# Performance work log

Measured on AMD Instinct MI355X. Metric: run time of the kernel, lower is better.

## Reference

```python
import jax, jax.numpy as jnp
import numpy as np

N = 100000   # num_nodes
E = 1600000  # num_edges (avg degree 16)
D = 64       # embed_channels
C = 16       # num_classes
EPSILON = 0.1  # AntiSymmetricConv step size (PyG default)
GAMMA = 0.1    # AntiSymmetricConv diffusion strength (PyG default)


def setup_inputs() -> dict:
    key = jax.random.key(0)
    ks = jax.random.split(key, 9)
    s = 1.0 / np.sqrt(D)
    return {
        "edge_index": jax.random.randint(ks[0], (2, E), 0, N, dtype=jnp.int32),
        "embed_w": jax.random.normal(ks[1], (N, D), dtype=jnp.float32) * 0.1,
        "W_rel": jax.random.normal(ks[2], (D, D), dtype=jnp.float32) * s,   # GraphConv lin_rel weight
        "b_rel": jax.random.normal(ks[3], (D,), dtype=jnp.float32) * s,     # GraphConv lin_rel bias
        "W_root": jax.random.normal(ks[4], (D, D), dtype=jnp.float32) * s,  # GraphConv lin_root weight (no bias)
        "W_anti": jax.random.normal(ks[5], (D, D), dtype=jnp.float32) * s,  # AntiSymmetricConv W
        "b_anti": jax.random.normal(ks[6], (D,), dtype=jnp.float32) * s,    # AntiSymmetricConv bias
        "W_lin": jax.random.normal(ks[7], (C, D), dtype=jnp.float32) * s,   # lin2 weight
        "b_lin": jax.random.normal(ks[8], (C,), dtype=jnp.float32) * s,     # lin2 bias
    }


def reference(edge_index, embed_w, W_rel, b_rel, W_root, W_anti, b_anti, W_lin, b_lin):
    x = embed_w  # [N, D] node features = embedding table
    src, dst = edge_index[0], edge_index[1]
    # phi = GraphConv with 'add' aggregation: lin_rel(sum_j x_j) + lin_root(x)
    agg = jax.ops.segment_sum(x[src], dst, num_segments=N)  # [N, D] sparse gather+scatter-add
    h = agg @ W_rel.T + b_rel + x @ W_root.T
    # antisymmetric weight: W - W^T - gamma * I
    aW = W_anti - W_anti.T - GAMMA * jnp.eye(D, dtype=x.dtype)
    h = x @ aW.T + h + b_anti
    h = jnp.tanh(h)                       # default act of AntiSymmetricConv
    x = x + EPSILON * h                   # single iteration (num_iters=1 default)
    # dropout p=0.0 -> identity
    out = jax.nn.sigmoid(x @ W_lin.T + b_lin)  # [N, C]
    return out
```

## Files before the change

kernel.cpp:

```cpp
#include <hip/hip_runtime.h>

#define DD 64
#define CC 16
#define EPSILON 0.1f
#define GAMMA 0.1f
#define BSH 6
#define BSZ 64
#define CAP 1280
#define MAXBK 2048
#define PAD 65
#define PADW 65
#define CSH 10
#define MAXNC 128
#define CAPC 20480
#define L1CHUNK 2048
#define L1THR 512
#define NSLICE 8
#define SRTSZ 2560

typedef float v2f __attribute__((ext_vector_type(2)));

__global__ __launch_bounds__(L1THR) void bin_coarse_conv(
        const int* __restrict__ ei, int* __restrict__ gcntc,
        unsigned* __restrict__ binned_c, int E,
        const float* __restrict__ x, unsigned* __restrict__ x_q, int N) {
    __shared__ unsigned sorted[SRTSZ];
    __shared__ unsigned char bkt[SRTSZ];
    __shared__ int hist[MAXNC], ph[MAXNC], base[MAXNC], cur[MAXNC], gbase[MAXNC];
    __shared__ int mtot;
    const int t = threadIdx.x;
    if (t < MAXNC) hist[t] = 0;
    __syncthreads();
    const int e0 = blockIdx.x * L1CHUNK;
    unsigned ent[L1CHUNK / L1THR];
    int cbk[L1CHUNK / L1THR];
#pragma unroll
    for (int i = 0; i < L1CHUNK / L1THR; ++i) {
        int e = e0 + t + L1THR * i;
        cbk[i] = -1;
        if (e < E) {
            int src = ei[e], dst = ei[E + e];
            cbk[i] = dst >> CSH;
            ent[i] = (unsigned)src | ((unsigned)(dst & ((1 << CSH) - 1)) << 17);
            atomicAdd(&hist[cbk[i]], 1);
        }
    }
    __syncthreads();
    if (t < MAXNC) { ph[t] = (hist[t] + 3) & ~3; cur[t] = ph[t]; }
    __syncthreads();
    for (int off = 1; off < MAXNC; off <<= 1) {
        int v = 0;
        if (t < MAXNC && t >= off) v = cur[t - off];
        __syncthreads();
        if (t < MAXNC) cur[t] += v;
        __syncthreads();
    }
    if (t < MAXNC) {
        base[t] = cur[t] - ph[t];
        if (t == MAXNC - 1) mtot = cur[t];
        cur[t] = base[t];
    }
    __syncthreads();
#pragma unroll
    for (int i = 0; i < L1CHUNK / L1THR; ++i)
        if (cbk[i] >= 0) {
            int pos = atomicAdd(&cur[cbk[i]], 1);
            sorted[pos] = ent[i];
            bkt[pos] = (unsigned char)cbk[i];
        }
    __syncthreads();
    if (t < MAXNC) {
        int b0 = base[t] + hist[t], b1 = base[t] + ph[t];
        for (int p = b0; p < b1; ++p) {
            sorted[p] = 0xFFFFFFFFu;
            bkt[p] = (unsigned char)t;
        }
        gbase[t] = ph[t] ? atomicAdd(&gcntc[t], ph[t]) : 0;
    }
    __syncthreads();
    const int m = mtot;
    for (int j4 = 4 * t; j4 < m; j4 += 4 * L1THR) {
        int cb = bkt[j4];
        int gp = gbase[cb] + (j4 - base[cb]);
        if (gp + 4 <= CAPC) {
            uint4 v = *(const uint4*)&sorted[j4];
            *(uint4*)&binned_c[(size_t)cb * CAPC + gp] = v;
        }
    }
    const float4* x4 = (const float4*)x;
    const int M = N * (DD / 4);
    const int G = gridDim.x * L1THR;
    for (int i = blockIdx.x * L1THR + t; i < M; i += G) {
        float4 a = x4[i];
        int r = __builtin_amdgcn_cvt_pk_fp8_f32(a.x, a.y, 0, false);
        r = __builtin_amdgcn_cvt_pk_fp8_f32(a.z, a.w, r, true);
        x_q[i] = (unsigned)r;
    }
}

__global__ __launch_bounds__(256) void bin_fine_w(
        const int* __restrict__ gcntc, const unsigned* __restrict__ binned_c,
        int* __restrict__ gcnt, unsigned* __restrict__ binned,
        const float* __restrict__ Wrel, const float* __restrict__ Wroot,
        const float* __restrict__ Wanti, const float* __restrict__ brel,
        const float* __restrict__ banti,
        float* __restrict__ B_g, float* __restrict__ bc) {
    const int t = threadIdx.x;
    if (blockIdx.x == gridDim.x - 1) {
        for (int idx = t; idx < 128 * 64; idx += 256) {
            int k = idx >> 6, d = idx & 63;
            float v;
            if (k < 64) {
                v = Wrel[d * 64 + k];
            } else {
                int j = k - 64;
                v = Wroot[d * 64 + j] + Wanti[d * 64 + j] - Wanti[j * 64 + d];
                if (d == j) v -= GAMMA;
            }
            B_g[idx] = v;
        }
        if (t < 64) bc[t] = brel[t] + banti[t];
        return;
    }
    __shared__ int hist[16];
    __shared__ int hbase[16];
    const int c = blockIdx.x >> 3, s = blockIdx.x & (NSLICE - 1);
    int cnt = gcntc[c];
    if (cnt > CAPC) cnt = CAPC;
    const int per = (cnt + NSLICE - 1) / NSLICE;
    const int i0 = s * per;
    int i1 = i0 + per;
    if (i1 > cnt) i1 = cnt;
    if (t < 16) hist[t] = 0;
    __syncthreads();
    const unsigned* bcp = binned_c + (size_t)c * CAPC;
    unsigned ent[10];
#pragma unroll
    for (int j = 0; j < 10; ++j) {
        int i = i0 + t + j * 256;
        ent[j] = (i < i1) ? bcp[i] : 0xFFFFFFFFu;
        if (ent[j] != 0xFFFFFFFFu) atomicAdd(&hist[ent[j] >> (17 + BSH)], 1);
    }
    __syncthreads();
    if (t < 16) {
        hbase[t] = hist[t] ? atomicAdd(&gcnt[c * 16 + t], hist[t]) : 0;
        hist[t] = 0;
    }
    __syncthreads();
#pragma unroll
    for (int j = 0; j < 10; ++j) {
        if (ent[j] != 0xFFFFFFFFu) {
            unsigned dstc = ent[j] >> 17;
            int f = dstc >> BSH;
            int pos = hbase[f] + atomicAdd(&hist[f], 1);
            if (pos < CAP)
                binned[(size_t)(c * 16 + f) * CAP + pos] =
                    (ent[j] & 0x1FFFF) | ((dstc & (BSZ - 1)) << 17);
        }
    }
}

__global__ __launch_bounds__(512, 8) void mega(
        const float* __restrict__ x, const unsigned* __restrict__ x_q,
        const int* __restrict__ gcnt, const unsigned* __restrict__ binned,
        const float* __restrict__ B_g, const float* __restrict__ bc,
        const float* __restrict__ Wlin, const float* __restrict__ blin,
        float* __restrict__ out, int N) {
    __shared__ float R0[BSZ * PAD];
    __shared__ float wl_sh[CC * PADW];
    __shared__ int csr[CAP];
    __shared__ int deg[BSZ], offs[BSZ], cur[BSZ];

    const int t = threadIdx.x;
    const int b = blockIdx.x;
    const int nb0 = b << BSH;
    int cnt = gcnt[b];
    if (cnt > CAP) cnt = CAP;
    const unsigned* bl = binned + (size_t)b * CAP;

#pragma unroll
    for (int i = 0; i < 2; ++i) {
        int idx = t + 512 * i;
        wl_sh[(idx >> 6) * PADW + (idx & 63)] = Wlin[idx];
    }
    if (t < BSZ) deg[t] = 0;
    __syncthreads();
    for (int i = t; i < cnt; i += 512) atomicAdd(&deg[bl[i] >> 17], 1);
    __syncthreads();
    if (t < BSZ) offs[t] = deg[t];
    __syncthreads();
    for (int off = 1; off < BSZ; off <<= 1) {
        int v = 0;
        if (t < BSZ && t >= off) v = offs[t - off];
        __syncthreads();
        if (t < BSZ) offs[t] += v;
        __syncthreads();
    }
    if (t < BSZ) {
        int ex = offs[t] - deg[t];
        offs[t] = ex;
        cur[t] = ex;
    }
    __syncthreads();
    for (int i = t; i < cnt; i += 512) {
        unsigned en = bl[i];
        int pos = atomicAdd(&cur[en >> 17], 1);
        csr[pos] = (int)(en & 0x1FFFF);
    }
    __syncthreads();

    {
        const int g = t >> 3, q = t & 7;
        const uint2* xq2 = (const uint2*)x_q;
        const int i0 = offs[g], dc = deg[g];
        float a0[8], a1[8];
#pragma unroll
        for (int r = 0; r < 8; ++r) { a0[r] = 0.f; a1[r] = 0.f; }
        int i = 0;
        for (; i + 2 <= dc; i += 2) {
            int s0 = csr[i0 + i], s1 = csr[i0 + i + 1];
            uint2 v0 = xq2[s0 * 8 + q];
            uint2 v1 = xq2[s1 * 8 + q];
            v2f f;
            f = __builtin_amdgcn_cvt_pk_f32_fp8(v0.x, false); a0[0] += f.x; a0[1] += f.y;
            f = __builtin_amdgcn_cvt_pk_f32_fp8(v0.x, true);  a0[2] += f.x; a0[3] += f.y;
            f = __builtin_amdgcn_cvt_pk_f32_fp8(v0.y, false); a0[4] += f.x; a0[5] += f.y;
            f = __builtin_amdgcn_cvt_pk_f32_fp8(v0.y, true);  a0[6] += f.x; a0[7] += f.y;
            f = __builtin_amdgcn_cvt_pk_f32_fp8(v1.x, false); a1[0] += f.x; a1[1] += f.y;
            f = __builtin_amdgcn_cvt_pk_f32_fp8(v1.x, true);  a1[2] += f.x; a1[3] += f.y;
            f = __builtin_amdgcn_cvt_pk_f32_fp8(v1.y, false); a1[4] += f.x; a1[5] += f.y;
            f = __builtin_amdgcn_cvt_pk_f32_fp8(v1.y, true);  a1[6] += f.x; a1[7] += f.y;
        }
        if (i < dc) {
            int s0 = csr[i0 + i];
            uint2 v0 = xq2[s0 * 8 + q];
            v2f f;
            f = __builtin_amdgcn_cvt_pk_f32_fp8(v0.x, false); a0[0] += f.x; a0[1] += f.y;
            f = __builtin_amdgcn_cvt_pk_f32_fp8(v0.x, true);  a0[2] += f.x; a0[3] += f.y;
            f = __builtin_amdgcn_cvt_pk_f32_fp8(v0.y, false); a0[4] += f.x; a0[5] += f.y;
            f = __builtin_amdgcn_cvt_pk_f32_fp8(v0.y, true);  a0[6] += f.x; a0[7] += f.y;
        }
        float* row = &R0[g * PAD + 8 * q];
#pragma unroll
        for (int r = 0; r < 8; ++r) row[r] = a0[r] + a1[r];
    }
    __syncthreads();

    const int nl = t & 63;
    const int dg = __builtin_amdgcn_readfirstlane(t >> 6);
    float acc[8];
#pragma unroll
    for (int j = 0; j < 8; ++j) acc[j] = 0.f;
#pragma unroll 8
    for (int k = 0; k < DD; ++k) {
        float a = R0[nl * PAD + k];
        const float* Bk = &B_g[k * DD + dg * 8];
#pragma unroll
        for (int j = 0; j < 8; ++j) acc[j] = fmaf(a, Bk[j], acc[j]);
    }
    __syncthreads();

    {
        int nn = N - nb0;
        if (nn > BSZ) nn = BSZ;
        const float4* x4 = (const float4*)x;
        for (int idx = t; idx < nn * 16; idx += 512) {
            float4 v = x4[nb0 * 16 + idx];
            float* row = &R0[(idx >> 4) * PAD + (idx & 15) * 4];
            row[0] = v.x; row[1] = v.y; row[2] = v.z; row[3] = v.w;
        }
    }
    __syncthreads();

#pragma unroll 8
    for (int k = 0; k < DD; ++k) {
        float a = R0[nl * PAD + k];
        const float* Bk = &B_g[(DD + k) * DD + dg * 8];
#pragma unroll
        for (int j = 0; j < 8; ++j) acc[j] = fmaf(a, Bk[j], acc[j]);
    }

#pragma unroll
    for (int j = 0; j < 8; ++j) {
        int d = dg * 8 + j;
        float h = acc[j] + bc[d];
        float e2 = __expf(2.0f * h);
        float th = 1.0f - 2.0f / (e2 + 1.0f);
        acc[j] = R0[nl * PAD + d] + EPSILON * th;
    }
    __syncthreads();
#pragma unroll
    for (int j = 0; j < 8; ++j) R0[nl * PAD + dg * 8 + j] = acc[j];
    __syncthreads();

    {
        const int g = t >> 3, q = t & 7;
        const int n = nb0 + g;
        if (n < N) {
            float p0 = blin[2 * q], p1 = blin[2 * q + 1];
#pragma unroll 8
            for (int d = 0; d < DD; ++d) {
                float xv = R0[g * PAD + d];
                p0 = fmaf(xv, wl_sh[(2 * q) * PADW + d], p0);
                p1 = fmaf(xv, wl_sh[(2 * q + 1) * PADW + d], p1);
            }
            float2 o;
            o.x = 1.0f / (1.0f + __expf(-p0));
            o.y = 1.0f / (1.0f + __expf(-p1));
            *(float2*)(out + (size_t)n * CC + 2 * q) = o;
        }
    }
}

extern "C" void kernel_launch(void* const* d_in, const int* in_sizes, int n_in,
                              void* d_out, int out_size, void* d_ws, size_t ws_size,
                              hipStream_t stream) {
    const int*   ei    = (const int*)d_in[0];
    const float* x     = (const float*)d_in[1];
    const float* Wrel  = (const float*)d_in[2];
    const float* brel  = (const float*)d_in[3];
    const float* Wroot = (const float*)d_in[4];
    const float* Wanti = (const float*)d_in[5];
    const float* banti = (const float*)d_in[6];
    const float* Wlin  = (const float*)d_in[7];
    const float* blin  = (const float*)d_in[8];
    float* out = (float*)d_out;

    const int E = in_sizes[0] / 2;
    const int N = in_sizes[1] / DD;
    const int NC = (N + (1 << CSH) - 1) >> CSH;

    unsigned* x_q = (unsigned*)d_ws;
    unsigned* binned_c = x_q + (size_t)N * (DD / 4);
    unsigned* binned = binned_c + (size_t)MAXNC * CAPC;
    int*   gcntc = (int*)(binned + (size_t)MAXBK * CAP);
    int*   gcnt  = gcntc + MAXNC;
    float* B_g   = (float*)(gcnt + MAXBK);
    float* bc    = B_g + 128 * 64;

    hipMemsetAsync(gcntc, 0, (MAXNC + MAXBK) * sizeof(int), stream);
    bin_coarse_conv<<<(E + L1CHUNK - 1) / L1CHUNK, L1THR, 0, stream>>>(
        ei, gcntc, binned_c, E, x, x_q, N);
    bin_fine_w<<<NC * NSLICE + 1, 256, 0, stream>>>(
        gcntc, binned_c, gcnt, binned, Wrel, Wroot, Wanti, brel, banti, B_g, bc);
    mega<<<NC * 16, 512, 0, stream>>>(x, x_q, gcnt, binned, B_g, bc, Wlin, blin, out, N);
}
```

Before: 173.6 us.

## Drop fine binning kernel; filter coarse bins per block inside mega

Removes the second binning pass. Each mega block now scans its whole coarse bin (about 16 fine blocks' worth of edges) and keeps only the entries for its own 64-node block, using a wave ballot to compact them into shared memory. The weight-matrix preparation moves into the first kernel, the coarse counters are padded to avoid sharing cache lines, and block indices are interleaved so blocks from different coarse bins run concurrently. This saves one launch and one global write/read of the binned edges, but makes each block read roughly 16 times more edge data from L2 and adds shared-memory staging.

```diff
diff --git a/kernel.cpp b/kernel.cpp
--- a/kernel.cpp
+++ b/kernel.cpp
@@ -7,15 +7,14 @@
 #define BSH 6
 #define BSZ 64
 #define CAP 1280
-#define MAXBK 2048
 #define PAD 65
 #define PADW 65
 #define CSH 10
 #define MAXNC 128
+#define CPAD 16
 #define CAPC 20480
 #define L1CHUNK 2048
 #define L1THR 512
-#define NSLICE 8
 #define SRTSZ 2560
 
 typedef float v2f __attribute__((ext_vector_type(2)));
@@ -23,7 +22,11 @@
 __global__ __launch_bounds__(L1THR) void bin_coarse_conv(
         const int* __restrict__ ei, int* __restrict__ gcntc,
         unsigned* __restrict__ binned_c, int E,
-        const float* __restrict__ x, unsigned* __restrict__ x_q, int N) {
+        const float* __restrict__ x, unsigned* __restrict__ x_q, int N,
+        const float* __restrict__ Wrel, const float* __restrict__ Wroot,
+        const float* __restrict__ Wanti, const float* __restrict__ brel,
+        const float* __restrict__ banti,
+        float* __restrict__ B_g, float* __restrict__ bc) {
     __shared__ unsigned sorted[SRTSZ];
     __shared__ unsigned char bkt[SRTSZ];
     __shared__ int hist[MAXNC], ph[MAXNC], base[MAXNC], cur[MAXNC], gbase[MAXNC];
@@ -75,7 +78,7 @@
             sorted[p] = 0xFFFFFFFFu;
             bkt[p] = (unsigned char)t;
         }
-        gbase[t] = ph[t] ? atomicAdd(&gcntc[t], ph[t]) : 0;
+        gbase[t] = ph[t] ? atomicAdd(&gcntc[t * CPAD], ph[t]) : 0;
     }
     __syncthreads();
     const int m = mtot;
@@ -87,27 +90,8 @@
             *(uint4*)&binned_c[(size_t)cb * CAPC + gp] = v;
         }
     }
-    const float4* x4 = (const float4*)x;
-    const int M = N * (DD / 4);
-    const int G = gridDim.x * L1THR;
-    for (int i = blockIdx.x * L1THR + t; i < M; i += G) {
-        float4 a = x4[i];
-        int r = __builtin_amdgcn_cvt_pk_fp8_f32(a.x, a.y, 0, false);
-        r = __builtin_amdgcn_cvt_pk_fp8_f32(a.z, a.w, r, true);
-        x_q[i] = (unsigned)r;
-    }
-}
-
-__global__ __launch_bounds__(256) void bin_fine_w(
-        const int* __restrict__ gcntc, const unsigned* __restrict__ binned_c,
-        int* __restrict__ gcnt, unsigned* __restrict__ binned,
-        const float* __restrict__ Wrel, const float* __restrict__ Wroot,
-        const float* __restrict__ Wanti, const float* __restrict__ brel,
-        const float* __restrict__ banti,
-        float* __restrict__ B_g, float* __restrict__ bc) {
-    const int t = threadIdx.x;
-    if (blockIdx.x == gridDim.x - 1) {
-        for (int idx = t; idx < 128 * 64; idx += 256) {
+    if (blockIdx.x == 0) {
+        for (int idx = t; idx < 128 * 64; idx += L1THR) {
             int k = idx >> 6, d = idx & 63;
             float v;
             if (k < 64) {
@@ -120,72 +104,78 @@
             B_g[idx] = v;
         }
         if (t < 64) bc[t] = brel[t] + banti[t];
-        return;
-    }
-    __shared__ int hist[16];
-    __shared__ int hbase[16];
-    const int c = blockIdx.x >> 3, s = blockIdx.x & (NSLICE - 1);
-    int cnt = gcntc[c];
-    if (cnt > CAPC) cnt = CAPC;
-    const int per = (cnt + NSLICE - 1) / NSLICE;
-    const int i0 = s * per;
-    int i1 = i0 + per;
-    if (i1 > cnt) i1 = cnt;
-    if (t < 16) hist[t] = 0;
-    __syncthreads();
-    const unsigned* bcp = binned_c + (size_t)c * CAPC;
-    unsigned ent[10];
-#pragma unroll
-    for (int j = 0; j < 10; ++j) {
-        int i = i0 + t + j * 256;
-        ent[j] = (i < i1) ? bcp[i] : 0xFFFFFFFFu;
-        if (ent[j] != 0xFFFFFFFFu) atomicAdd(&hist[ent[j] >> (17 + BSH)], 1);
-    }
-    __syncthreads();
-    if (t < 16) {
-        hbase[t] = hist[t] ? atomicAdd(&gcnt[c * 16 + t], hist[t]) : 0;
-        hist[t] = 0;
-    }
-    __syncthreads();
-#pragma unroll
-    for (int j = 0; j < 10; ++j) {
-        if (ent[j] != 0xFFFFFFFFu) {
-            unsigned dstc = ent[j] >> 17;
-            int f = dstc >> BSH;
-            int pos = hbase[f] + atomicAdd(&hist[f], 1);
-            if (pos < CAP)
-                binned[(size_t)(c * 16 + f) * CAP + pos] =
-                    (ent[j] & 0x1FFFF) | ((dstc & (BSZ - 1)) << 17);
-        }
+    }
+    const float4* x4 = (const float4*)x;
+    const int M = N * (DD / 4);
+    const int G = gridDim.x * L1THR;
+    for (int i = blockIdx.x * L1THR + t; i < M; i += G) {
+        float4 a = x4[i];
+        int r = __builtin_amdgcn_cvt_pk_fp8_f32(a.x, a.y, 0, false);
+        r = __builtin_amdgcn_cvt_pk_fp8_f32(a.z, a.w, r, true);
+        x_q[i] = (unsigned)r;
     }
 }
 
 __global__ __launch_bounds__(512, 8) void mega(
         const float* __restrict__ x, const unsigned* __restrict__ x_q,
-        const int* __restrict__ gcnt, const unsigned* __restrict__ binned,
+        const int* __restrict__ gcntc, const unsigned* __restrict__ binned_c,
         const float* __restrict__ B_g, const float* __restrict__ bc,
         const float* __restrict__ Wlin, const float* __restrict__ blin,
-        float* __restrict__ out, int N) {
+        float* __restrict__ out, int N, int NC) {
     __shared__ float R0[BSZ * PAD];
     __shared__ float wl_sh[CC * PADW];
     __shared__ int csr[CAP];
+    __shared__ int stage[CAP];
     __shared__ int deg[BSZ], offs[BSZ], cur[BSZ];
+    __shared__ int ns;
 
     const int t = threadIdx.x;
-    const int b = blockIdx.x;
+    const int r = blockIdx.x & 7, mm = blockIdx.x >> 3;
+    const int c = ((mm >> 4) << 3) + r;
+    const int k = mm & 15;
+    if (c >= NC) return;
+    const int b = c * 16 + k;
     const int nb0 = b << BSH;
-    int cnt = gcnt[b];
-    if (cnt > CAP) cnt = CAP;
-    const unsigned* bl = binned + (size_t)b * CAP;
+
+    int cntc = gcntc[c * CPAD];
+    if (cntc > CAPC) cntc = CAPC;
+    const unsigned* bcp = binned_c + (size_t)c * CAPC;
 
 #pragma unroll
     for (int i = 0; i < 2; ++i) {
         int idx = t + 512 * i;
         wl_sh[(idx >> 6) * PADW + (idx & 63)] = Wlin[idx];
     }
+    if (t == 0) ns = 0;
     if (t < BSZ) deg[t] = 0;
     __syncthreads();
-    for (int i = t; i < cnt; i += 512) atomicAdd(&deg[bl[i] >> 17], 1);
+
+    {
+        const int lane = t & 63;
+        for (int i4 = 4 * t; i4 < cntc; i4 += 4 * 512) {
+            uint4 v = *(const uint4*)&bcp[i4];
+#pragma unroll
+            for (int jj = 0; jj < 4; ++jj) {
+                unsigned en = (jj == 0) ? v.x : (jj == 1) ? v.y : (jj == 2) ? v.z : v.w;
+                bool mt = (en < (1u << 27)) && (((en >> (17 + BSH)) & 15u) == (unsigned)k);
+                unsigned long long msk = __ballot(mt);
+                if (mt) {
+                    int ldr = __ffsll((long long)msk) - 1;
+                    int bpos = 0;
+                    if (lane == ldr) bpos = atomicAdd(&ns, __popcll(msk));
+                    bpos = __shfl(bpos, ldr);
+                    int pos = bpos + __popcll(msk & ((1ull << lane) - 1ull));
+                    if (pos < CAP)
+                        stage[pos] = (int)((en & 0x1FFFF) | (((en >> 17) & 63u) << 17));
+                }
+            }
+        }
+    }
+    __syncthreads();
+    int cnt = ns;
+    if (cnt > CAP) cnt = CAP;
+
+    for (int i = t; i < cnt; i += 512) atomicAdd(&deg[stage[i] >> 17], 1);
     __syncthreads();
     if (t < BSZ) offs[t] = deg[t];
     __syncthreads();
@@ -203,9 +193,9 @@
     }
     __syncthreads();
     for (int i = t; i < cnt; i += 512) {
-        unsigned en = bl[i];
+        int en = stage[i];
         int pos = atomicAdd(&cur[en >> 17], 1);
-        csr[pos] = (int)(en & 0x1FFFF);
+        csr[pos] = en & 0x1FFFF;
     }
     __syncthreads();
 
@@ -215,7 +205,7 @@
         const int i0 = offs[g], dc = deg[g];
         float a0[8], a1[8];
 #pragma unroll
-        for (int r = 0; r < 8; ++r) { a0[r] = 0.f; a1[r] = 0.f; }
+        for (int rr = 0; rr < 8; ++rr) { a0[rr] = 0.f; a1[rr] = 0.f; }
         int i = 0;
         for (; i + 2 <= dc; i += 2) {
             int s0 = csr[i0 + i], s1 = csr[i0 + i + 1];
@@ -242,7 +232,7 @@
         }
         float* row = &R0[g * PAD + 8 * q];
 #pragma unroll
-        for (int r = 0; r < 8; ++r) row[r] = a0[r] + a1[r];
+        for (int rr = 0; rr < 8; ++rr) row[rr] = a0[rr] + a1[rr];
     }
     __syncthreads();
 
@@ -252,9 +242,9 @@
 #pragma unroll
     for (int j = 0; j < 8; ++j) acc[j] = 0.f;
 #pragma unroll 8
-    for (int k = 0; k < DD; ++k) {
-        float a = R0[nl * PAD + k];
-        const float* Bk = &B_g[k * DD + dg * 8];
+    for (int kk = 0; kk < DD; ++kk) {
+        float a = R0[nl * PAD + kk];
+        const float* Bk = &B_g[kk * DD + dg * 8];
 #pragma unroll
         for (int j = 0; j < 8; ++j) acc[j] = fmaf(a, Bk[j], acc[j]);
     }
@@ -266,16 +256,16 @@
         const float4* x4 = (const float4*)x;
         for (int idx = t; idx < nn * 16; idx += 512) {
             float4 v = x4[nb0 * 16 + idx];
-            float* row = &R0[(idx >> 4) * PAD + (idx & 15) * 4];
-            row[0] = v.x; row[1] = v.y; row[2] = v.z; row[3] = v.w;
+            float* rw = &R0[(idx >> 4) * PAD + (idx & 15) * 4];
+            rw[0] = v.x; rw[1] = v.y; rw[2] = v.z; rw[3] = v.w;
         }
     }
     __syncthreads();
 
 #pragma unroll 8
-    for (int k = 0; k < DD; ++k) {
-        float a = R0[nl * PAD + k];
-        const float* Bk = &B_g[(DD + k) * DD + dg * 8];
+    for (int kk = 0; kk < DD; ++kk) {
+        float a = R0[nl * PAD + kk];
+        const float* Bk = &B_g[(DD + kk) * DD + dg * 8];
 #pragma unroll
         for (int j = 0; j < 8; ++j) acc[j] = fmaf(a, Bk[j], acc[j]);
     }
@@ -332,16 +322,15 @@
 
     unsigned* x_q = (unsigned*)d_ws;
     unsigned* binned_c = x_q + (size_t)N * (DD / 4);
-    unsigned* binned = binned_c + (size_t)MAXNC * CAPC;
-    int*   gcntc = (int*)(binned + (size_t)MAXBK * CAP);
-    int*   gcnt  = gcntc + MAXNC;
-    float* B_g   = (float*)(gcnt + MAXBK);
+    int*   gcntc = (int*)(binned_c + (size_t)MAXNC * CAPC);
+    float* B_g   = (float*)(gcntc + MAXNC * CPAD);
     float* bc    = B_g + 128 * 64;
 
-    hipMemsetAsync(gcntc, 0, (MAXNC + MAXBK) * sizeof(int), stream);
+    hipMemsetAsync(gcntc, 0, MAXNC * CPAD * sizeof(int), stream);
     bin_coarse_conv<<<(E + L1CHUNK - 1) / L1CHUNK, L1THR, 0, stream>>>(
-        ei, gcntc, binned_c, E, x, x_q, N);
-    bin_fine_w<<<NC * NSLICE + 1, 256, 0, stream>>>(
-        gcntc, binned_c, gcnt, binned, Wrel, Wroot, Wanti, brel, banti, B_g, bc);
-    mega<<<NC * 16, 512, 0, stream>>>(x, x_q, gcnt, binned, B_g, bc, Wlin, blin, out, N);
+        ei, gcntc, binned_c, E, x, x_q, N,
+        Wrel, Wroot, Wanti, brel, banti, B_g, bc);
+    const int gb = ((NC + 7) / 8) * 8 * 16;
+    mega<<<gb, 512, 0, stream>>>(x, x_q, gcntc, binned_c, B_g, bc, Wlin, blin,
+                                 out, N, NC);
 }
```

After: 184.5 us. 6.3% more time.
